# Performance work log

Measured on AMD Instinct MI355X. Metric: run time of the kernel, lower is better.

The kernel has to match this reference:

```python
import jax, jax.numpy as jnp
import numpy as np

S, N, L, B = 200000, 250000, 64, 64


def setup_inputs() -> dict:
    key = jax.random.key(0)
    k = jax.random.split(key, 7)
    return {
        "We_m": jax.random.normal(k[0], (S, L), jnp.float32) * 0.02,
        "be_m": jax.random.normal(k[1], (L,), jnp.float32) * 0.02,
        "Wd_m": jax.random.normal(k[2], (L, S), jnp.float32) * 0.02,
        "bd_m": jax.random.normal(k[3], (S,), jnp.float32) * 0.02,
        "x": jax.random.normal(k[4], (B, N), jnp.float32),
        "nn_n": jax.random.randint(k[5], (N,), 0, S),  # nearest master node for each new node
        "nn_m": jax.random.randint(k[6], (S,), 0, N),  # nearest new node for each master node
    }


def _reshape_weights(We_m, be_m, Wd_m, bd_m, nn_n, nn_m):
    # Vectorized equivalent of GFN_AE.reshape_weights(expand=True, agglomerate=True,
    # update_master=False, eval mode).
    s, l = We_m.shape
    n = nn_n.shape[0]
    # Expand: new node pt_n is "added" iff nn_m[nn_n[pt_n]] != pt_n.
    added = (nn_m[nn_n] != jnp.arange(n)).astype(We_m.dtype)  # [N]
    # Sequential We_i[pt_m] *= c/(c+1) collapses to division by (c_m + 1),
    # c_m = number of added new nodes whose nearest master node is m.
    c_m = jax.ops.segment_sum(added, nn_n, num_segments=s)  # [S]
    We_s = We_m / (c_m + 1.0)[:, None]  # scaled master encoder rows
    # Appended row i (for added node pt_n, src m = nn_n[pt_n]) equals We_s[m],
    # Wd column / bd entry copied from m; its nn_m_ext entry is pt_n itself.
    # Agglomerate: We_n sums contributors, Wd_n/bd_n take the running mean (= plain mean).
    We_n = jax.ops.segment_sum(We_s, nn_m, num_segments=n) + added[:, None] * We_s[nn_n]
    WdT = Wd_m.T  # [S, L]
    cnt = jax.ops.segment_sum(jnp.ones((s,), We_m.dtype), nn_m, num_segments=n) + added
    denom = jnp.maximum(cnt, 1.0)
    Wd_n = ((jax.ops.segment_sum(WdT, nn_m, num_segments=n) + added[:, None] * WdT[nn_n]) / denom[:, None]).T  # [L, N]
    bd_n = (jax.ops.segment_sum(bd_m, nn_m, num_segments=n) + added * bd_m[nn_n]) / denom  # [N]
    return We_n, Wd_n, bd_n


def reference(We_m, be_m, Wd_m, bd_m, x, nn_n, nn_m):
    We_n, Wd_n, bd_n = _reshape_weights(We_m, be_m, Wd_m, bd_m, nn_n, nn_m)
    z = x @ We_n + be_m            # encode: [B, N] x [N, L]
    out = z @ Wd_n + bd_n          # decode: [B, L] x [L, N]
    return out
```

## Files before the change

kernel.cpp:

```cpp
#include <hip/hip_runtime.h>

constexpr int S_ = 200000;
constexpr int N_ = 250000;

constexpr int NCHUNK = (N_ + 63) / 64;
constexpr int ENC_BLOCKS = (NCHUNK + 3) / 4;
constexpr int WEN_BLOCKS = NCHUNK * 2;
constexpr int DEC_BLOCKS = (N_ + 31) / 32;

typedef __attribute__((ext_vector_type(8))) short bf16x8;
typedef __attribute__((ext_vector_type(4))) float f32x4;
typedef __attribute__((ext_vector_type(4))) unsigned short us4;
typedef __attribute__((ext_vector_type(8))) unsigned short us8;

__global__ void k_added_counts(const int* __restrict__ nn_n, const int* __restrict__ nn_m,
                               int* __restrict__ added, int* __restrict__ c_m,
                               int* __restrict__ ecnt) {
    int i = blockIdx.x * 256 + threadIdx.x;
    if (i < N_) {
        int m = nn_n[i];
        int a = (nn_m[m] != i) ? 1 : 0;
        added[i] = a;
        if (a) {
            atomicAdd(&c_m[m], 1);
            atomicAdd(&ecnt[i], 1);
        }
    }
    if (i < S_) {
        atomicAdd(&ecnt[nn_m[i]], 1);
    }
}

__global__ void k_scan_blocksum(const int* __restrict__ ecnt, int* __restrict__ bsum) {
    __shared__ int sd[256];
    int b = blockIdx.x, t = threadIdx.x;
    int base = b * 1024 + t * 4;
    int s = 0;
#pragma unroll
    for (int k = 0; k < 4; k++) { int idx = base + k; if (idx < N_) s += ecnt[idx]; }
    sd[t] = s;
    __syncthreads();
    for (int off = 128; off > 0; off >>= 1) {
        if (t < off) sd[t] += sd[t + off];
        __syncthreads();
    }
    if (t == 0) bsum[b] = sd[0];
}

__global__ void k_scan_apply(const int* __restrict__ ecnt, const int* __restrict__ bsum,
                             int* __restrict__ offs) {
    __shared__ int sd[256];
    __shared__ int sp[256];
    int b = blockIdx.x, t = threadIdx.x;
    sp[t] = (t < b) ? bsum[t] : 0;
    __syncthreads();
    for (int off = 128; off > 0; off >>= 1) {
        if (t < off) sp[t] += sp[t + off];
        __syncthreads();
    }
    int prev = sp[0];

    int base = b * 1024 + t * 4;
    int v[4]; int s = 0;
#pragma unroll
    for (int k = 0; k < 4; k++) { int idx = base + k; v[k] = (idx < N_) ? ecnt[idx] : 0; s += v[k]; }
    sd[t] = s;
    __syncthreads();
    for (int off = 1; off < 256; off <<= 1) {
        int xv = (t >= off) ? sd[t - off] : 0;
        __syncthreads();
        sd[t] += xv;
        __syncthreads();
    }
    int run = prev + sd[t] - s;
#pragma unroll
    for (int k = 0; k < 4; k++) {
        int idx = base + k;
        if (idx < N_) offs[idx] = run;
        run += v[k];
    }
}

__global__ void k_fill(const int* __restrict__ nn_m, const int* __restrict__ nn_n,
                       const int* __restrict__ added, const int* __restrict__ offs,
                       int* __restrict__ fill, int* __restrict__ elist) {
    int i = blockIdx.x * 256 + threadIdx.x;
    if (i < S_) {
        int j = nn_m[i];
        int p = atomicAdd(&fill[j], 1);
        elist[offs[j] + p] = i;
    }
    if (i < N_ && added[i]) {
        int p = atomicAdd(&fill[i], 1);
        elist[offs[i] + p] = nn_n[i];
    }
}

__global__ __launch_bounds__(256) void k_wen(
        const float* __restrict__ We_m, const int* __restrict__ c_m,
        const int* __restrict__ ecnt, const int* __restrict__ offs,
        const int* __restrict__ elist, unsigned short* __restrict__ Wf) {
    __shared__ unsigned short sw[4096];
    int t = threadIdx.x;
    int lane = t & 63;
    int wv = __builtin_amdgcn_readfirstlane(t >> 6);
    int b = blockIdx.x;
    int jb = b * 32 + wv * 8;
    int c[8], o[8];
    float acc[8];
#pragma unroll
    for (int s = 0; s < 8; s++) {
        int j = jb + s;
        bool v = (j < N_);
        c[s] = v ? __builtin_amdgcn_readfirstlane(ecnt[j]) : 0;
        o[s] = v ? __builtin_amdgcn_readfirstlane(offs[j]) : 0;
        acc[s] = 0.f;
    }
    int cmax = 0;
#pragma unroll
    for (int s = 0; s < 8; s++) cmax = max(cmax, c[s]);
    for (int q = 0; q < cmax; q++) {
        int mm[8]; float sc[8];
#pragma unroll
        for (int s = 0; s < 8; s++) {
            int cl = max(c[s] - 1, 0);
            int p = o[s] + min(q, cl);
            int e = __builtin_amdgcn_readfirstlane(elist[p]);
            bool valid = (q < c[s]);
            mm[s] = valid ? e : 0;
        }
#pragma unroll
        for (int s = 0; s < 8; s++) {
            int cm = __builtin_amdgcn_readfirstlane(c_m[mm[s]]);
            bool valid = (q < c[s]);
            sc[s] = valid ? 1.0f / (float)(cm + 1) : 0.0f;
        }
        float row[8];
#pragma unroll
        for (int s = 0; s < 8; s++)
            row[s] = We_m[(size_t)mm[s] * 64 + lane];
#pragma unroll
        for (int s = 0; s < 8; s++)
            acc[s] += row[s] * sc[s];
    }

    int ct = lane >> 4, l15 = lane & 15;
    us8 hv, lv;
#pragma unroll
    for (int s = 0; s < 8; s++) {
        float v = acc[s];
        unsigned u = __float_as_uint(v);
        hv[s] = (unsigned short)(u >> 16);
        float r = v - __uint_as_float(u & 0xffff0000u);
        lv[s] = (unsigned short)(__float_as_uint(r) >> 16);
    }
    int base = ct * 1024 + (l15 + 16 * wv) * 8;
    *(us8*)&sw[base]       = hv;
    *(us8*)&sw[base + 512] = lv;
    __syncthreads();
    int ch = b >> 1, sH = b & 1;
    size_t R = ((size_t)ch * 2 + sH) * 4096;
#pragma unroll
    for (int r = 0; r < 2; r++) {
        int idx = r * 2048 + t * 8;
        *(us8*)(Wf + R + idx) = *(const us8*)&sw[idx];
    }
}

__global__ __launch_bounds__(256) void k_encode(const float* __restrict__ x,
        const unsigned short* __restrict__ Wf, float* __restrict__ zp2) {
    int t = threadIdx.x;
    int lane = t & 63;
    int wv = t >> 6;
    int mrow = lane & 15;
    int kq = lane >> 4;
    const float* xbase = x + (size_t)(wv * 16 + mrow) * N_ + kq * 8;
    f32x4 acc[4];
#pragma unroll
    for (int ct = 0; ct < 4; ct++) acc[ct] = (f32x4){0.f, 0.f, 0.f, 0.f};

    for (int cc = 0; cc < 4; cc++) {
        int c = blockIdx.x * 4 + cc;
        if (c >= NCHUNK) break;
        int n0 = c * 64;
#pragma unroll
        for (int s = 0; s < 2; s++) {
            float av[8];
            if (n0 + s * 32 + kq * 8 + 8 <= N_) {
                float4 a0 = *(const float4*)(xbase + n0 + s * 32);
                float4 a1 = *(const float4*)(xbase + n0 + s * 32 + 4);
                av[0] = a0.x; av[1] = a0.y; av[2] = a0.z; av[3] = a0.w;
                av[4] = a1.x; av[5] = a1.y; av[6] = a1.z; av[7] = a1.w;
            } else {
#pragma unroll
                for (int i = 0; i < 8; i++) av[i] = 0.f;
            }
            const bf16x8* bp = (const bf16x8*)Wf + ((size_t)c * 2 + s) * 512 + lane;
            bf16x8 bh[4], bl[4];
#pragma unroll
            for (int ct = 0; ct < 4; ct++) {
                bh[ct] = bp[ct * 128];
                bl[ct] = bp[ct * 128 + 64];
            }
            bf16x8 ah, al;
#pragma unroll
            for (int i = 0; i < 8; i++) {
                float v = av[i];
                unsigned u = __float_as_uint(v);
                ah[i] = (short)(u >> 16);
                float r = v - __uint_as_float(u & 0xffff0000u);
                al[i] = (short)(__float_as_uint(r) >> 16);
            }
#pragma unroll
            for (int ct = 0; ct < 4; ct++) {
                acc[ct] = __builtin_amdgcn_mfma_f32_16x16x32_bf16(ah, bh[ct], acc[ct], 0, 0, 0);
                acc[ct] = __builtin_amdgcn_mfma_f32_16x16x32_bf16(al, bh[ct], acc[ct], 0, 0, 0);
                acc[ct] = __builtin_amdgcn_mfma_f32_16x16x32_bf16(ah, bl[ct], acc[ct], 0, 0, 0);
            }
        }
    }

    int row = blockIdx.x & 63;
    float* zr = zp2 + row * 4096;
#pragma unroll
    for (int ct = 0; ct < 4; ct++) {
#pragma unroll
        for (int r = 0; r < 4; r++) {
            int b = wv * 16 + kq * 4 + r;
            int l = ct * 16 + mrow;
            atomicAdd(&zr[b * 64 + l], acc[ct][r]);
        }
    }
}

__global__ void k_zred(const float* __restrict__ zp2, const float* __restrict__ be_m,
                       float* __restrict__ z2g) {
    int slot = blockIdx.x * 256 + threadIdx.x;
    float s = 0.f;
    for (int r = 0; r < 64; r++) s += zp2[r * 4096 + slot];
    int b = slot >> 6, l = slot & 63;
    z2g[l * 64 + b] = s + be_m[l];
}

__global__ __launch_bounds__(256) void k_pmat(
        const float* __restrict__ Wd_m, const float* __restrict__ bd_m,
        const float* __restrict__ z2g, float* __restrict__ P) {
    __shared__ float ws[64 * 64];
    int t = threadIdx.x;
    int m0 = blockIdx.x * 64;
#pragma unroll
    for (int r = 0; r < 4; r++) {
        int flat = r * 256 + t;
        int l = flat >> 4;
        int c4 = flat & 15;
        float4 v = *(const float4*)&Wd_m[(size_t)l * S_ + m0 + c4 * 4];
        *(float4*)&ws[l * 64 + c4 * 4] = v;
    }
    __syncthreads();

    int m = t & 63;
    int bg = __builtin_amdgcn_readfirstlane(t >> 6);
    float bd = bd_m[m0 + m];
    float acc[16];
#pragma unroll
    for (int q = 0; q < 16; q++) acc[q] = bd;
    const float* zb = z2g + bg * 16;
#pragma unroll 4
    for (int l = 0; l < 64; l++) {
        float w = ws[l * 64 + m];
        const float* zr = zb + l * 64;
#pragma unroll
        for (int q = 0; q < 16; q++) acc[q] += w * zr[q];
    }

    float4* Pv = (float4*)&P[(size_t)(m0 + m) * 64 + bg * 16];
#pragma unroll
    for (int q4 = 0; q4 < 4; q4++)
        Pv[q4] = make_float4(acc[q4 * 4 + 0], acc[q4 * 4 + 1],
                             acc[q4 * 4 + 2], acc[q4 * 4 + 3]);
}

__global__ __launch_bounds__(256) void k_decode(const float* __restrict__ P,
        const int* __restrict__ ecnt, const int* __restrict__ offs,
        const int* __restrict__ elist, float* __restrict__ out) {
    __shared__ float tile[32][65];
    int t = threadIdx.x;
    int wv = __builtin_amdgcn_readfirstlane(t >> 6);
    int lane = t & 63;
    int j0 = blockIdx.x * 32;
    int jb = j0 + wv * 8;
    int c[8], o[8];
    float acc[8];
#pragma unroll
    for (int s = 0; s < 8; s++) {
        int j = jb + s;
        bool v = (j < N_);
        c[s] = v ? __builtin_amdgcn_readfirstlane(ecnt[j]) : 0;
        o[s] = v ? __builtin_amdgcn_readfirstlane(offs[j]) : 0;
        acc[s] = 0.f;
    }
    int cmax = 0;
#pragma unroll
    for (int s = 0; s < 8; s++) cmax = max(cmax, c[s]);
    for (int q = 0; q < cmax; q++) {
        int mm[8]; float sc[8];
#pragma unroll
        for (int s = 0; s < 8; s++) {
            int cl = max(c[s] - 1, 0);
            int p = o[s] + min(q, cl);
            int e = __builtin_amdgcn_readfirstlane(elist[p]);
            bool valid = (q < c[s]);
            mm[s] = valid ? e : 0;
            sc[s] = valid ? 1.0f : 0.0f;
        }
        float row[8];
#pragma unroll
        for (int s = 0; s < 8; s++)
            row[s] = P[(size_t)mm[s] * 64 + lane];
#pragma unroll
        for (int s = 0; s < 8; s++)
            acc[s] += row[s] * sc[s];
    }
#pragma unroll
    for (int s = 0; s < 8; s++) {
        int cc = (c[s] > 1) ? c[s] : 1;
        tile[wv * 8 + s][lane] = acc[s] * (1.0f / (float)cc);
    }
    __syncthreads();
#pragma unroll
    for (int r = 0; r < 8; r++) {
        int b = r * 8 + (t >> 5);
        int j = j0 + (t & 31);
        if (j < N_) out[(size_t)b * N_ + j] = tile[t & 31][b];
    }
}

extern "C" void kernel_launch(void* const* d_in, const int* in_sizes, int n_in,
                              void* d_out, int out_size, void* d_ws, size_t ws_size,
                              hipStream_t stream) {
    const float* We_m = (const float*)d_in[0];
    const float* be_m = (const float*)d_in[1];
    const float* Wd_m = (const float*)d_in[2];
    const float* bd_m = (const float*)d_in[3];
    const float* x    = (const float*)d_in[4];
    const int*   nn_n = (const int*)d_in[5];
    const int*   nn_m = (const int*)d_in[6];
    float* out = (float*)d_out;
    char* ws = (char*)d_ws;

    unsigned short* Wf = (unsigned short*)(ws + 0);
    float* P     = (float*)(ws + 0);
    int*   c_m   = (int*)(ws + 64012288);
    int*   ecnt  = (int*)(ws + 64812288);
    int*   fill  = (int*)(ws + 65812288);
    int*   added = (int*)(ws + 66812288);
    int*   offs  = (int*)(ws + 67812288);
    int*   elist = (int*)(ws + 68812288);
    float* zp2   = (float*)(ws + 70812288);
    float* z2g   = (float*)(ws + 71860864);
    int*   bsum  = (int*)(ws + 71877248);

    hipMemsetAsync(ws + 64012288, 0, 2800000, stream);
    hipMemsetAsync(zp2, 0, 1048576, stream);

    k_added_counts<<<977, 256, 0, stream>>>(nn_n, nn_m, added, c_m, ecnt);
    k_scan_blocksum<<<245, 256, 0, stream>>>(ecnt, bsum);
    k_scan_apply<<<245, 256, 0, stream>>>(ecnt, bsum, offs);
    k_fill<<<977, 256, 0, stream>>>(nn_m, nn_n, added, offs, fill, elist);
    k_wen<<<WEN_BLOCKS, 256, 0, stream>>>(We_m, c_m, ecnt, offs, elist, Wf);
    k_encode<<<ENC_BLOCKS, 256, 0, stream>>>(x, Wf, zp2);
    k_zred<<<16, 256, 0, stream>>>(zp2, be_m, z2g);
    k_pmat<<<3125, 256, 0, stream>>>(Wd_m, bd_m, z2g, P);
    k_decode<<<DEC_BLOCKS, 256, 0, stream>>>(P, ecnt, offs, elist, out);
}
```

Baseline: 361.4 us.

## Pack master scale count into edge list and prefetch next edge entries

The fill kernel now stores each master's c_m count in the upper bits of its edge-list entry, above an 18-bit index. This lets k_wen drop its dependent c_m gather and compute the scale with a fast reciprocal. Both k_wen and k_decode now software-pipeline the edge-list reads, loading the next iteration's entries before using the current ones, which shortens the serial load chain. The packing limits indices to 18 bits and counts to the remaining bits, which fits S and N here. rcpf is slightly less exact than a true division.

New measurement: 350.7 us. -3.0%, faster.

```diff
diff --git a/kernel.cpp b/kernel.cpp
--- a/kernel.cpp
+++ b/kernel.cpp
@@ -7,6 +7,8 @@
 constexpr int ENC_BLOCKS = (NCHUNK + 3) / 4;
 constexpr int WEN_BLOCKS = NCHUNK * 2;
 constexpr int DEC_BLOCKS = (N_ + 31) / 32;
+
+constexpr int EMASK = 0x3FFFF;
 
 typedef __attribute__((ext_vector_type(8))) short bf16x8;
 typedef __attribute__((ext_vector_type(4))) float f32x4;
@@ -83,21 +85,23 @@
 
 __global__ void k_fill(const int* __restrict__ nn_m, const int* __restrict__ nn_n,
                        const int* __restrict__ added, const int* __restrict__ offs,
+                       const int* __restrict__ c_m,
                        int* __restrict__ fill, int* __restrict__ elist) {
     int i = blockIdx.x * 256 + threadIdx.x;
     if (i < S_) {
         int j = nn_m[i];
         int p = atomicAdd(&fill[j], 1);
-        elist[offs[j] + p] = i;
+        elist[offs[j] + p] = i | (c_m[i] << 18);
     }
     if (i < N_ && added[i]) {
+        int m = nn_n[i];
         int p = atomicAdd(&fill[i], 1);
-        elist[offs[i] + p] = nn_n[i];
+        elist[offs[i] + p] = m | (c_m[m] << 18);
     }
 }
 
 __global__ __launch_bounds__(256) void k_wen(
-        const float* __restrict__ We_m, const int* __restrict__ c_m,
+        const float* __restrict__ We_m,
         const int* __restrict__ ecnt, const int* __restrict__ offs,
         const int* __restrict__ elist, unsigned short* __restrict__ Wf) {
     __shared__ unsigned short sw[4096];
@@ -106,7 +110,7 @@
     int wv = __builtin_amdgcn_readfirstlane(t >> 6);
     int b = blockIdx.x;
     int jb = b * 32 + wv * 8;
-    int c[8], o[8];
+    int c[8], o[8], cl[8];
     float acc[8];
 #pragma unroll
     for (int s = 0; s < 8; s++) {
@@ -114,34 +118,43 @@
         bool v = (j < N_);
         c[s] = v ? __builtin_amdgcn_readfirstlane(ecnt[j]) : 0;
         o[s] = v ? __builtin_amdgcn_readfirstlane(offs[j]) : 0;
+        cl[s] = max(c[s] - 1, 0);
         acc[s] = 0.f;
     }
     int cmax = 0;
 #pragma unroll
     for (int s = 0; s < 8; s++) cmax = max(cmax, c[s]);
-    for (int q = 0; q < cmax; q++) {
-        int mm[8]; float sc[8];
-#pragma unroll
-        for (int s = 0; s < 8; s++) {
-            int cl = max(c[s] - 1, 0);
-            int p = o[s] + min(q, cl);
-            int e = __builtin_amdgcn_readfirstlane(elist[p]);
-            bool valid = (q < c[s]);
-            mm[s] = valid ? e : 0;
+
+    if (cmax > 0) {
+        int e[8];
+#pragma unroll
+        for (int s = 0; s < 8; s++)
+            e[s] = __builtin_amdgcn_readfirstlane(elist[o[s]]);
+        for (int q = 0; q < cmax; q++) {
+            int en[8];
+#pragma unroll
+            for (int s = 0; s < 8; s++) {
+                int p = o[s] + min(q + 1, cl[s]);
+                en[s] = __builtin_amdgcn_readfirstlane(elist[p]);
+            }
+            int mm[8]; float sc[8];
+#pragma unroll
+            for (int s = 0; s < 8; s++) {
+                bool valid = (q < c[s]);
+                mm[s] = valid ? (e[s] & EMASK) : 0;
+                float r = __builtin_amdgcn_rcpf((float)((e[s] >> 18) + 1));
+                sc[s] = valid ? r : 0.0f;
+            }
+            float row[8];
+#pragma unroll
+            for (int s = 0; s < 8; s++)
+                row[s] = We_m[(size_t)mm[s] * 64 + lane];
+#pragma unroll
+            for (int s = 0; s < 8; s++)
+                acc[s] += row[s] * sc[s];
+#pragma unroll
+            for (int s = 0; s < 8; s++) e[s] = en[s];
         }
-#pragma unroll
-        for (int s = 0; s < 8; s++) {
-            int cm = __builtin_amdgcn_readfirstlane(c_m[mm[s]]);
-            bool valid = (q < c[s]);
-            sc[s] = valid ? 1.0f / (float)(cm + 1) : 0.0f;
-        }
-        float row[8];
-#pragma unroll
-        for (int s = 0; s < 8; s++)
-            row[s] = We_m[(size_t)mm[s] * 64 + lane];
-#pragma unroll
-        for (int s = 0; s < 8; s++)
-            acc[s] += row[s] * sc[s];
     }
 
     int ct = lane >> 4, l15 = lane & 15;
@@ -289,7 +302,7 @@
     int lane = t & 63;
     int j0 = blockIdx.x * 32;
     int jb = j0 + wv * 8;
-    int c[8], o[8];
+    int c[8], o[8], cl[8];
     float acc[8];
 #pragma unroll
     for (int s = 0; s < 8; s++) {
@@ -297,29 +310,42 @@
         bool v = (j < N_);
         c[s] = v ? __builtin_amdgcn_readfirstlane(ecnt[j]) : 0;
         o[s] = v ? __builtin_amdgcn_readfirstlane(offs[j]) : 0;
+        cl[s] = max(c[s] - 1, 0);
         acc[s] = 0.f;
     }
     int cmax = 0;
 #pragma unroll
     for (int s = 0; s < 8; s++) cmax = max(cmax, c[s]);
-    for (int q = 0; q < cmax; q++) {
-        int mm[8]; float sc[8];
-#pragma unroll
-        for (int s = 0; s < 8; s++) {
-            int cl = max(c[s] - 1, 0);
-            int p = o[s] + min(q, cl);
-            int e = __builtin_amdgcn_readfirstlane(elist[p]);
-            bool valid = (q < c[s]);
-            mm[s] = valid ? e : 0;
-            sc[s] = valid ? 1.0f : 0.0f;
+
+    if (cmax > 0) {
+        int e[8];
+#pragma unroll
+        for (int s = 0; s < 8; s++)
+            e[s] = __builtin_amdgcn_readfirstlane(elist[o[s]]);
+        for (int q = 0; q < cmax; q++) {
+            int en[8];
+#pragma unroll
+            for (int s = 0; s < 8; s++) {
+                int p = o[s] + min(q + 1, cl[s]);
+                en[s] = __builtin_amdgcn_readfirstlane(elist[p]);
+            }
+            int mm[8]; float sc[8];
+#pragma unroll
+            for (int s = 0; s < 8; s++) {
+                bool valid = (q < c[s]);
+                mm[s] = valid ? (e[s] & EMASK) : 0;
+                sc[s] = valid ? 1.0f : 0.0f;
+            }
+            float row[8];
+#pragma unroll
+            for (int s = 0; s < 8; s++)
+                row[s] = P[(size_t)mm[s] * 64 + lane];
+#pragma unroll
+            for (int s = 0; s < 8; s++)
+                acc[s] += row[s] * sc[s];
+#pragma unroll
+            for (int s = 0; s < 8; s++) e[s] = en[s];
         }
-        float row[8];
-#pragma unroll
-        for (int s = 0; s < 8; s++)
-            row[s] = P[(size_t)mm[s] * 64 + lane];
-#pragma unroll
-        for (int s = 0; s < 8; s++)
-            acc[s] += row[s] * sc[s];
     }
 #pragma unroll
     for (int s = 0; s < 8; s++) {
@@ -366,8 +392,8 @@
     k_added_counts<<<977, 256, 0, stream>>>(nn_n, nn_m, added, c_m, ecnt);
     k_scan_blocksum<<<245, 256, 0, stream>>>(ecnt, bsum);
     k_scan_apply<<<245, 256, 0, stream>>>(ecnt, bsum, offs);
-    k_fill<<<977, 256, 0, stream>>>(nn_m, nn_n, added, offs, fill, elist);
-    k_wen<<<WEN_BLOCKS, 256, 0, stream>>>(We_m, c_m, ecnt, offs, elist, Wf);
+    k_fill<<<977, 256, 0, stream>>>(nn_m, nn_n, added, offs, c_m, fill, elist);
+    k_wen<<<WEN_BLOCKS, 256, 0, stream>>>(We_m, ecnt, offs, elist, Wf);
     k_encode<<<ENC_BLOCKS, 256, 0, stream>>>(x, Wf, zp2);
     k_zred<<<16, 256, 0, stream>>>(zp2, be_m, z2g);
     k_pmat<<<3125, 256, 0, stream>>>(Wd_m, bd_m, z2g, P);
```
